# Kernel tuning notes

Hardware: AMD Instinct MI355X
Metric: run time of the kernel (lower is better)

## Reference

```python
import jax, jax.numpy as jnp
import numpy as np

RADIUS = 0.1
NUM_POINT = 1024  # M centroids
SAMPLE_NUM = 32   # K neighbors per ball


def fps(xyz, m):
    """D-FPS farthest point sampling. xyz: (B,N,3) -> idx (B,m) int32."""
    B, N, _ = xyz.shape

    def step(carry, _):
        mind, far = carry  # mind (B,N), far (B,)
        centroid = jnp.take_along_axis(xyz, far[:, None, None], axis=1)  # (B,1,3)
        d = jnp.sum((xyz - centroid) ** 2, axis=-1)  # (B,N)
        mind = jnp.minimum(mind, d)
        nxt = jnp.argmax(mind, axis=1).astype(jnp.int32)
        return (mind, nxt), far

    init = (jnp.full((B, N), jnp.inf, xyz.dtype), jnp.zeros((B,), jnp.int32))
    _, idx = jax.lax.scan(step, init, None, length=m)
    return jnp.transpose(idx)  # (B,m)


def ball_query(new_xyz, xyz, radius, k):
    """First-k points within radius of each centroid, padded with first hit.
    new_xyz (B,M,3), xyz (B,N,3) -> (B,M,k) int32."""
    N = xyz.shape[1]
    d2 = jnp.sum((new_xyz[:, :, None, :] - xyz[:, None, :, :]) ** 2, axis=-1)  # (B,M,N)
    order = jnp.where(d2 < radius * radius, jnp.arange(N, dtype=jnp.int32)[None, None, :], N)
    neg, pos = jax.lax.top_k(-order, k)  # k smallest 'order' values -> first-k in-ball indices
    valid = (-neg) < N
    return jnp.where(valid, pos, pos[..., :1])


def setup_inputs() -> dict:
    key = jax.random.key(0)
    ks = jax.random.split(key, 12)
    B, N, C = 4, 16384, 64
    Cin = C + 3  # use_xyz=True
    points_xyz = jax.random.uniform(ks[0], (B, N, 3), dtype=jnp.float32)
    features = jax.random.normal(ks[1], (B, C, N), dtype=jnp.float32)
    s = lambda fan: 1.0 / np.sqrt(fan)
    inp = {
        "points_xyz": points_xyz,
        "features": features,
        "Wa": jax.random.normal(ks[2], (128, Cin), jnp.float32) * s(Cin),
        "ba": jnp.zeros((128,), jnp.float32),
        "Wb": jax.random.normal(ks[3], (128, 128), jnp.float32) * s(128),
        "bb": jnp.zeros((128,), jnp.float32),
        "Ws": jax.random.normal(ks[4], (128, Cin), jnp.float32) * s(Cin),
        "bs": jnp.zeros((128,), jnp.float32),
        "Wc": jax.random.normal(ks[5], (512, 128), jnp.float32) * s(128),
        "bc": jnp.zeros((512,), jnp.float32),
        "Wd": jax.random.normal(ks[6], (128, 512), jnp.float32) * s(512),
        "bd": jnp.zeros((128,), jnp.float32),
    }
    return inp


def _conv1x1(W, b, x):
    # pointwise conv over (B,C,M,K)
    return jnp.einsum('oc,bcmk->bomk', W, x) + b[None, :, None, None]


def reference(points_xyz, features, Wa, ba, Wb, bb, Ws, bs, Wc, bc, Wd, bd):
    idx = fps(points_xyz, NUM_POINT)  # (B,M)
    new_xyz = jnp.take_along_axis(points_xyz, idx[:, :, None], axis=1)  # (B,M,3)
    nidx = ball_query(new_xyz, points_xyz, RADIUS, SAMPLE_NUM)  # (B,M,K)
    # gather and relativize grouped xyz; gather grouped features
    grouped_xyz = jax.vmap(lambda p, i: p[i])(points_xyz, nidx) - new_xyz[:, :, None, :]  # (B,M,K,3)
    gfeat = jax.vmap(lambda f, i: f[:, i])(features, nidx)  # (B,C,M,K)
    g = jnp.concatenate([jnp.transpose(grouped_xyz, (0, 3, 1, 2)), gfeat], axis=1)  # (B,3+C,M,K)
    # mlp + shortcut residual + relu
    h = _conv1x1(Wb, bb, jax.nn.relu(_conv1x1(Wa, ba, g)))
    h = jax.nn.relu(h + _conv1x1(Ws, bs, g))
    # inverted mlp + identity residual + relu
    inv = _conv1x1(Wd, bd, jax.nn.relu(_conv1x1(Wc, bc, h)))
    out = jax.nn.relu(inv + h)
    pooled = jnp.max(out, axis=-1)  # max pool over K -> (B,128,M)
    return new_xyz, pooled, idx
```

## Files before the change

kernel.cpp:

```cpp
#include <hip/hip_runtime.h>

#define N_PTS   16384
#define M_CENT  1024
#define K_SMP   32
#define C_FEAT  64
#define NCELL   512

using bf16x8 = __attribute__((ext_vector_type(8))) short;
using s16x4  = __attribute__((ext_vector_type(4))) short;
using f32x4  = __attribute__((ext_vector_type(4))) float;

__device__ inline short f2bf(float f) {
    unsigned u = __float_as_uint(f);
    u += 0x7fffu + ((u >> 16) & 1u);
    return (short)(u >> 16);
}

__device__ inline unsigned long long shfl_xor_u64(unsigned long long v, int m) {
    int lo = (int)(unsigned int)v;
    int hi = (int)(unsigned int)(v >> 32);
    lo = __shfl_xor(lo, m);
    hi = __shfl_xor(hi, m);
    return ((unsigned long long)(unsigned int)hi << 32) | (unsigned int)lo;
}

__device__ inline int part3(int v) {
    return (v & 1) | ((v & 2) << 2) | ((v & 4) << 4);
}
__device__ inline int cell_of(float x, float y, float z) {
    int xi = (int)(x * 8.0f); xi = xi < 0 ? 0 : (xi > 7 ? 7 : xi);
    int yi = (int)(y * 8.0f); yi = yi < 0 ? 0 : (yi > 7 ? 7 : yi);
    int zi = (int)(z * 8.0f); zi = zi < 0 ? 0 : (zi > 7 ? 7 : zi);
    return part3(xi) | (part3(yi) << 1) | (part3(zi) << 2);
}

__global__ __launch_bounds__(1024) void hist_kernel(
    const float* __restrict__ xyz, int* __restrict__ ghist)
{
    __shared__ int h[NCELL];
    const int b = blockIdx.x, tid = threadIdx.x;
    if (tid < NCELL) h[tid] = 0;
    __syncthreads();
    const float* P = xyz + (size_t)b * N_PTS * 3;
    for (int i = 0; i < 16; ++i) {
        const int p = tid + (i << 10);
        atomicAdd(&h[cell_of(P[p*3], P[p*3+1], P[p*3+2])], 1);
    }
    __syncthreads();
    if (tid < NCELL) ghist[b * NCELL + tid] = h[tid];
}

__global__ __launch_bounds__(NCELL) void scan_kernel(
    const int* __restrict__ ghist, int* __restrict__ gbase)
{
    __shared__ int h[NCELL];
    const int b = blockIdx.x, t = threadIdx.x;
    h[t] = ghist[b * NCELL + t];
    __syncthreads();
    int s = 0;
    for (int i = 0; i < t; ++i) s += h[i];
    gbase[b * NCELL + t] = s;
}

__global__ __launch_bounds__(1024) void scatter_kernel(
    const float* __restrict__ xyz, int* __restrict__ gbase,
    float4* __restrict__ gsxyz)
{
    const int b = blockIdx.x, tid = threadIdx.x;
    const float* P = xyz + (size_t)b * N_PTS * 3;
    for (int i = 0; i < 16; ++i) {
        const int p = tid + (i << 10);
        float x = P[p*3], y = P[p*3+1], z = P[p*3+2];
        int c = cell_of(x, y, z);
        int pos = atomicAdd(&gbase[b * NCELL + c], 1);
        gsxyz[(size_t)b * N_PTS + pos] = make_float4(x, y, z, __int_as_float(p));
    }
}

__global__ __launch_bounds__(1024) void fps_kernel(
    const float* __restrict__ xyz,
    const float4* __restrict__ gsxyz,
    float* __restrict__ newxyz_out,
    float* __restrict__ idxf_out)
{
#pragma clang fp contract(off)
    const int b = blockIdx.x, tid = threadIdx.x;
    const int wid = tid >> 6, lane = tid & 63;
    const float4* S = gsxyz + (size_t)b * N_PTS;

    float px[16], py[16], pz[16], mind[16];
    unsigned klo[16];
    float lox = 1e30f, hix = -1e30f, loy = 1e30f, hiy = -1e30f, loz = 1e30f, hiz = -1e30f;
#pragma unroll
    for (int i = 0; i < 16; ++i) {
        const float4 v = S[tid * 16 + i];
        px[i] = v.x; py[i] = v.y; pz[i] = v.z;
        const int orig = __float_as_int(v.w);
        klo[i] = ((unsigned)(16383 - orig) << 16) | (unsigned)(tid * 16 + i);
        mind[i] = __int_as_float(0x7f800000);
        lox = fminf(lox, v.x); hix = fmaxf(hix, v.x);
        loy = fminf(loy, v.y); hiy = fmaxf(hiy, v.y);
        loz = fminf(loz, v.z); hiz = fmaxf(hiz, v.z);
    }

    __shared__ unsigned long long wblk[2][16];

    const float* P = xyz + (size_t)b * N_PTS * 3;
    float cx = P[0], cy = P[1], cz = P[2];
    if (tid == 0) {
        idxf_out[b * M_CENT] = 0.0f;
        newxyz_out[(b * M_CENT) * 3 + 0] = cx;
        newxyz_out[(b * M_CENT) * 3 + 1] = cy;
        newxyz_out[(b * M_CENT) * 3 + 2] = cz;
    }
    __syncthreads();

    unsigned long long bkey = 0x7f80000000000000ull;
    unsigned long long wkey = 0x7f80000000000000ull;

    for (int j = 1; j < M_CENT; ++j) {
        const int par = j & 1;
        float tx = fmaxf(fmaxf(lox - cx, cx - hix), 0.0f);
        float ty = fmaxf(fmaxf(loy - cy, cy - hiy), 0.0f);
        float tz = fmaxf(fmaxf(loz - cz, cz - hiz), 0.0f);
        float lb = (tx * tx + ty * ty) + tz * tz;
        float lmax = __uint_as_float((unsigned)(bkey >> 32));
        bool need = (lb * 0.999985f) < lmax;

        if (__any(need)) {
            float bv = -1.0f;
#pragma unroll
            for (int i = 0; i < 16; ++i) {
                float dx = px[i] - cx;
                float dy = py[i] - cy;
                float dz = pz[i] - cz;
                float xx = dx * dx, yy = dy * dy, zz = dz * dz;
                float d  = (xx + yy) + zz;
                float mn = fminf(mind[i], d);
                mind[i] = mn;
                bv = fmaxf(bv, mn);
            }
            unsigned bk = 0u;
#pragma unroll
            for (int i = 0; i < 16; ++i)
                if (mind[i] == bv && klo[i] > bk) bk = klo[i];
            bkey = ((unsigned long long)__float_as_uint(bv) << 32) | bk;

            unsigned long long w = bkey;
#pragma unroll
            for (int off = 32; off >= 1; off >>= 1) {
                unsigned long long o = shfl_xor_u64(w, off);
                if (o > w) w = o;
            }
            wkey = w;
        }
        if (lane == 0) wblk[par][wid] = wkey;
        __syncthreads();

        unsigned long long k2 = wblk[par][lane & 15];
#pragma unroll
        for (int off = 8; off >= 1; off >>= 1) {
            unsigned long long o = shfl_xor_u64(k2, off);
            if (o > k2) k2 = o;
        }
        const unsigned int kl = (unsigned int)k2;
        const int sorted = (int)(kl & 0xFFFFu);
        const float4 wv = S[sorted];
        cx = wv.x; cy = wv.y; cz = wv.z;
        if (tid == 0) {
            const int orig = 16383 - (int)(kl >> 16);
            idxf_out[b * M_CENT + j] = (float)orig;
            newxyz_out[(b * M_CENT + j) * 3 + 0] = cx;
            newxyz_out[(b * M_CENT + j) * 3 + 1] = cy;
            newxyz_out[(b * M_CENT + j) * 3 + 2] = cz;
        }
    }
}

__global__ __launch_bounds__(256) void ball_kernel(
    const float* __restrict__ xyz,
    const float* __restrict__ newxyz,
    int* __restrict__ nidx)
{
#pragma clang fp contract(off)
    const float R2 = (float)(0.1 * 0.1);
    const int gw   = blockIdx.x * 4 + (threadIdx.x >> 6);
    const int lane = threadIdx.x & 63;
    const int b    = gw >> 10;
    const float* P = xyz + (size_t)b * N_PTS * 3;
    const float cx = newxyz[gw * 3 + 0];
    const float cy = newxyz[gw * 3 + 1];
    const float cz = newxyz[gw * 3 + 2];
    int* out = nidx + gw * K_SMP;

    int cnt = 0, first = -1;
    for (int base = 0; base < N_PTS; base += 64) {
        const int n = base + lane;
        float dx = P[n * 3 + 0] - cx;
        float dy = P[n * 3 + 1] - cy;
        float dz = P[n * 3 + 2] - cz;
        float xx = dx * dx, yy = dy * dy, zz = dz * dz;
        float d2 = (xx + yy) + zz;
        bool inb = d2 < R2;
        unsigned long long mask = __ballot(inb);
        if (mask) {
            if (first < 0) first = base + __ffsll(mask) - 1;
            int before = __popcll(mask & ((1ull << lane) - 1ull));
            int slot = cnt + before;
            if (inb && slot < K_SMP) out[slot] = n;
            cnt += __popcll(mask);
            if (cnt >= K_SMP) break;
        }
    }
    for (int s = cnt + lane; s < K_SMP; s += 64) out[s] = first;
}

__global__ void prep_w(const float* __restrict__ src, short* __restrict__ dst,
                       int OC, int IC, int ICP, int remap)
{
    int i = blockIdx.x * 256 + threadIdx.x;
    if (i >= OC * ICP) return;
    int oc = i / ICP, ic = i - oc * ICP;
    float v = 0.0f;
    if (remap) {
        if (ic < 64)      v = src[oc * IC + 3 + ic];
        else if (ic < 67) v = src[oc * IC + (ic - 64)];
    } else if (ic < IC)   v = src[oc * IC + ic];
    dst[i] = f2bf(v);
}

__global__ __launch_bounds__(256) void tfeat_kernel(
    const float* __restrict__ feat, float* __restrict__ featT)
{
    __shared__ float t[64][65];
    const int b = blockIdx.y;
    const int n0 = blockIdx.x * 64;
    for (int it = 0; it < 16; ++it) {
        int idx = it * 256 + threadIdx.x;
        int c = idx >> 6, n = idx & 63;
        t[c][n] = feat[((size_t)b * 64 + c) * N_PTS + n0 + n];
    }
    __syncthreads();
    for (int it = 0; it < 16; ++it) {
        int idx = it * 256 + threadIdx.x;
        int n = idx >> 6, c = idx & 63;
        featT[((size_t)b * N_PTS + n0 + n) * 64 + c] = t[c][n];
    }
}

__global__ __launch_bounds__(256, 2) void mlp_kernel(
    const float* __restrict__ xyz, const float* __restrict__ feat,
    const float* __restrict__ featT, int useT,
    const float* __restrict__ newxyz, const int* __restrict__ nidx,
    const short* __restrict__ WaB, const float* __restrict__ ba,
    const short* __restrict__ WbB, const float* __restrict__ bb,
    const short* __restrict__ WsB, const float* __restrict__ bs,
    const short* __restrict__ WcB, const float* __restrict__ bc,
    const short* __restrict__ WdB, const float* __restrict__ bd,
    float* __restrict__ pooled)
{
    __shared__ short Xt[64][104];
    __shared__ short Ht[64][136];
    __shared__ short Tt[64][136];

    const int tid = threadIdx.x;
    const int w = tid >> 6, l = tid & 63, l16 = l & 15, kg = l >> 4;
    const int cen0 = blockIdx.x * 2;
    const int b = cen0 >> 10;
    const int ocw = 32 * w;

    {
        const int col = tid >> 2, part = tid & 3;
        const int ci = cen0 + (col >> 5);
        const int nn = nidx[ci * K_SMP + (col & 31)];
        float v[16];
        if (useT) {
            const f32x4* src = (const f32x4*)(featT + ((size_t)b * N_PTS + nn) * 64 + part * 16);
            f32x4 f0 = src[0], f1 = src[1], f2 = src[2], f3 = src[3];
            v[0]=f0[0]; v[1]=f0[1]; v[2]=f0[2]; v[3]=f0[3];
            v[4]=f1[0]; v[5]=f1[1]; v[6]=f1[2]; v[7]=f1[3];
            v[8]=f2[0]; v[9]=f2[1]; v[10]=f2[2]; v[11]=f2[3];
            v[12]=f3[0]; v[13]=f3[1]; v[14]=f3[2]; v[15]=f3[3];
        } else {
            const float* F = feat + (size_t)b * C_FEAT * N_PTS + nn;
#pragma unroll
            for (int q = 0; q < 16; ++q) v[q] = F[(size_t)(part * 16 + q) * N_PTS];
        }
        bf16x8 h0, h1;
#pragma unroll
        for (int q = 0; q < 8; ++q) { h0[q] = f2bf(v[q]); h1[q] = f2bf(v[q + 8]); }
        *(bf16x8*)&Xt[col][part * 16]     = h0;
        *(bf16x8*)&Xt[col][part * 16 + 8] = h1;
        if (part == 0) {
            bf16x8 hx, z;
#pragma unroll
            for (int q = 0; q < 8; ++q) { hx[q] = 0; z[q] = 0; }
            hx[0] = f2bf(xyz[((size_t)b * N_PTS + nn) * 3 + 0] - newxyz[ci * 3 + 0]);
            hx[1] = f2bf(xyz[((size_t)b * N_PTS + nn) * 3 + 1] - newxyz[ci * 3 + 1]);
            hx[2] = f2bf(xyz[((size_t)b * N_PTS + nn) * 3 + 2] - newxyz[ci * 3 + 2]);
            *(bf16x8*)&Xt[col][64] = hx;
            *(bf16x8*)&Xt[col][72] = z;
            *(bf16x8*)&Xt[col][80] = z;
            *(bf16x8*)&Xt[col][88] = z;
        }
    }
    __syncthreads();

    f32x4 accA[2][4], accS[2][4];
#pragma unroll
    for (int o = 0; o < 2; ++o)
#pragma unroll
        for (int ct = 0; ct < 4; ++ct) {
#pragma unroll
            for (int r = 0; r < 4; ++r) { accA[o][ct][r] = 0.f; accS[o][ct][r] = 0.f; }
        }
#pragma unroll
    for (int k = 0; k < 3; ++k) {
        bf16x8 xb[4];
#pragma unroll
        for (int ct = 0; ct < 4; ++ct)
            xb[ct] = *(const bf16x8*)&Xt[ct * 16 + l16][k * 32 + kg * 8];
#pragma unroll
        for (int o = 0; o < 2; ++o) {
            const int row = ocw + o * 16 + l16;
            bf16x8 wa  = *(const bf16x8*)(WaB + row * 96 + k * 32 + kg * 8);
            bf16x8 wsv = *(const bf16x8*)(WsB + row * 96 + k * 32 + kg * 8);
#pragma unroll
            for (int ct = 0; ct < 4; ++ct) {
                accA[o][ct] = __builtin_amdgcn_mfma_f32_16x16x32_bf16(wa,  xb[ct], accA[o][ct], 0, 0, 0);
                accS[o][ct] = __builtin_amdgcn_mfma_f32_16x16x32_bf16(wsv, xb[ct], accS[o][ct], 0, 0, 0);
            }
        }
    }
#pragma unroll
    for (int o = 0; o < 2; ++o) {
        const f32x4 bav = *(const f32x4*)(ba + ocw + o * 16 + kg * 4);
#pragma unroll
        for (int ct = 0; ct < 4; ++ct) {
            s16x4 hv;
#pragma unroll
            for (int r = 0; r < 4; ++r) hv[r] = f2bf(fmaxf(accA[o][ct][r] + bav[r], 0.f));
            *(s16x4*)&Ht[ct * 16 + l16][ocw + o * 16 + kg * 4] = hv;
        }
    }
    __syncthreads();

    f32x4 accB[2][4];
#pragma unroll
    for (int o = 0; o < 2; ++o)
#pragma unroll
        for (int ct = 0; ct < 4; ++ct) {
#pragma unroll
            for (int r = 0; r < 4; ++r) accB[o][ct][r] = 0.f;
        }
#pragma unroll
    for (int k = 0; k < 4; ++k) {
        bf16x8 xb[4];
#pragma unroll
        for (int ct = 0; ct < 4; ++ct)
            xb[ct] = *(const bf16x8*)&Ht[ct * 16 + l16][k * 32 + kg * 8];
#pragma unroll
        for (int o = 0; o < 2; ++o) {
            const int row = ocw + o * 16 + l16;
            bf16x8 wbv = *(const bf16x8*)(WbB + row * 128 + k * 32 + kg * 8);
#pragma unroll
            for (int ct = 0; ct < 4; ++ct)
                accB[o][ct] = __builtin_amdgcn_mfma_f32_16x16x32_bf16(wbv, xb[ct], accB[o][ct], 0, 0, 0);
        }
    }
    f32x4 hreg[2][4];
#pragma unroll
    for (int o = 0; o < 2; ++o) {
        const f32x4 bbv = *(const f32x4*)(bb + ocw + o * 16 + kg * 4);
        const f32x4 bsv = *(const f32x4*)(bs + ocw + o * 16 + kg * 4);
#pragma unroll
        for (int ct = 0; ct < 4; ++ct) {
#pragma unroll
            for (int r = 0; r < 4; ++r)
                hreg[o][ct][r] = fmaxf((accB[o][ct][r] + bbv[r]) + (accS[o][ct][r] + bsv[r]), 0.f);
        }
    }
    __syncthreads();
#pragma unroll
    for (int o = 0; o < 2; ++o)
#pragma unroll
        for (int ct = 0; ct < 4; ++ct) {
            s16x4 hv;
#pragma unroll
            for (int r = 0; r < 4; ++r) hv[r] = f2bf(hreg[o][ct][r]);
            *(s16x4*)&Ht[ct * 16 + l16][ocw + o * 16 + kg * 4] = hv;
        }
    __syncthreads();

    f32x4 accD[2][4];
#pragma unroll
    for (int o = 0; o < 2; ++o)
#pragma unroll
        for (int ct = 0; ct < 4; ++ct) {
#pragma unroll
            for (int r = 0; r < 4; ++r) accD[o][ct][r] = 0.f;
        }
    for (int cc = 0; cc < 4; ++cc) {
        f32x4 accC[2][4];
#pragma unroll
        for (int o = 0; o < 2; ++o)
#pragma unroll
            for (int ct = 0; ct < 4; ++ct) {
#pragma unroll
                for (int r = 0; r < 4; ++r) accC[o][ct][r] = 0.f;
            }
#pragma unroll
        for (int k = 0; k < 4; ++k) {
            bf16x8 xb[4];
#pragma unroll
            for (int ct = 0; ct < 4; ++ct)
                xb[ct] = *(const bf16x8*)&Ht[ct * 16 + l16][k * 32 + kg * 8];
#pragma unroll
            for (int o = 0; o < 2; ++o) {
                const int row = cc * 128 + ocw + o * 16 + l16;
                bf16x8 wcv = *(const bf16x8*)(WcB + row * 128 + k * 32 + kg * 8);
#pragma unroll
                for (int ct = 0; ct < 4; ++ct)
                    accC[o][ct] = __builtin_amdgcn_mfma_f32_16x16x32_bf16(wcv, xb[ct], accC[o][ct], 0, 0, 0);
            }
        }
        __syncthreads();
#pragma unroll
        for (int o = 0; o < 2; ++o) {
            const f32x4 bcv = *(const f32x4*)(bc + cc * 128 + ocw + o * 16 + kg * 4);
#pragma unroll
            for (int ct = 0; ct < 4; ++ct) {
                s16x4 tv;
#pragma unroll
                for (int r = 0; r < 4; ++r) tv[r] = f2bf(fmaxf(accC[o][ct][r] + bcv[r], 0.f));
                *(s16x4*)&Tt[ct * 16 + l16][ocw + o * 16 + kg * 4] = tv;
            }
        }
        __syncthreads();
#pragma unroll
        for (int k = 0; k < 4; ++k) {
            bf16x8 tb[4];
#pragma unroll
            for (int ct = 0; ct < 4; ++ct)
                tb[ct] = *(const bf16x8*)&Tt[ct * 16 + l16][k * 32 + kg * 8];
#pragma unroll
            for (int o = 0; o < 2; ++o) {
                const int row = ocw + o * 16 + l16;
                bf16x8 wdv = *(const bf16x8*)(WdB + row * 512 + cc * 128 + k * 32 + kg * 8);
#pragma unroll
                for (int ct = 0; ct < 4; ++ct)
                    accD[o][ct] = __builtin_amdgcn_mfma_f32_16x16x32_bf16(wdv, tb[ct], accD[o][ct], 0, 0, 0);
            }
        }
    }

    const int m0 = cen0 & 1023;
#pragma unroll
    for (int o = 0; o < 2; ++o) {
        const f32x4 bdv = *(const f32x4*)(bd + ocw + o * 16 + kg * 4);
#pragma unroll
        for (int r = 0; r < 4; ++r) {
            float a0 = fmaxf((accD[o][0][r] + bdv[r]) + hreg[o][0][r], 0.f);
            float a1 = fmaxf((accD[o][1][r] + bdv[r]) + hreg[o][1][r], 0.f);
            float a2 = fmaxf((accD[o][2][r] + bdv[r]) + hreg[o][2][r], 0.f);
            float a3 = fmaxf((accD[o][3][r] + bdv[r]) + hreg[o][3][r], 0.f);
            float u0 = fmaxf(a0, a1), u1 = fmaxf(a2, a3);
#pragma unroll
            for (int off = 1; off < 16; off <<= 1) {
                u0 = fmaxf(u0, __shfl_xor(u0, off));
                u1 = fmaxf(u1, __shfl_xor(u1, off));
            }
            if (l16 == 0) {
                const int oc = ocw + o * 16 + kg * 4 + r;
                pooled[((size_t)b * 128 + oc) * 1024 + m0]     = u0;
                pooled[((size_t)b * 128 + oc) * 1024 + m0 + 1] = u1;
            }
        }
    }
}

extern "C" void kernel_launch(void* const* d_in, const int* in_sizes, int n_in,
                              void* d_out, int out_size, void* d_ws, size_t ws_size,
                              hipStream_t stream)
{
    const float* xyz  = (const float*)d_in[0];
    const float* feat = (const float*)d_in[1];
    const float* Wa = (const float*)d_in[2];   const float* ba = (const float*)d_in[3];
    const float* Wb = (const float*)d_in[4];   const float* bb = (const float*)d_in[5];
    const float* Ws = (const float*)d_in[6];   const float* bs = (const float*)d_in[7];
    const float* Wc = (const float*)d_in[8];   const float* bc = (const float*)d_in[9];
    const float* Wd = (const float*)d_in[10];  const float* bd = (const float*)d_in[11];

    float* out    = (float*)d_out;
    float* newxyz = out;
    float* pooled = out + 4 * 1024 * 3;
    float* idxf   = pooled + 4 * 128 * 1024;

    char* ws = (char*)d_ws;
    float4* gsxyz = (float4*)ws;
    int*    nidx  = (int*)ws;
    short* WaB = (short*)(ws + (1 << 20));
    short* WsB = WaB + 128 * 96;
    short* WbB = WsB + 128 * 96;
    short* WcB = WbB + 128 * 128;
    short* WdB = WcB + 512 * 128;
    int*   ghist = (int*)(WdB + 128 * 512);
    int*   gbase = ghist + 4 * NCELL;
    float* featT = (float*)(ws + (2 << 20));

    const size_t need = (size_t)(2 << 20) + (size_t)4 * N_PTS * 64 * 4;
    const int useT = (ws_size >= need) ? 1 : 0;

    prep_w<<<(128 *  96 + 255) / 256, 256, 0, stream>>>(Wa, WaB, 128,  67,  96, 1);
    prep_w<<<(128 *  96 + 255) / 256, 256, 0, stream>>>(Ws, WsB, 128,  67,  96, 1);
    prep_w<<<(128 * 128 + 255) / 256, 256, 0, stream>>>(Wb, WbB, 128, 128, 128, 0);
    prep_w<<<(512 * 128 + 255) / 256, 256, 0, stream>>>(Wc, WcB, 512, 128, 128, 0);
    prep_w<<<(128 * 512 + 255) / 256, 256, 0, stream>>>(Wd, WdB, 128, 512, 512, 0);
    if (useT) tfeat_kernel<<<dim3(N_PTS / 64, 4), 256, 0, stream>>>(feat, featT);

    hist_kernel   <<<4, 1024,  0, stream>>>(xyz, ghist);
    scan_kernel   <<<4, NCELL, 0, stream>>>(ghist, gbase);
    scatter_kernel<<<4, 1024,  0, stream>>>(xyz, gbase, gsxyz);

    fps_kernel<<<4, 1024, 0, stream>>>(xyz, gsxyz, newxyz, idxf);
    ball_kernel<<<1024, 256, 0, stream>>>(xyz, newxyz, nidx);
    mlp_kernel<<<2048, 256, 0, stream>>>(xyz, feat, featT, useT, newxyz, nidx,
                                         WaB, ba, WbB, bb, WsB, bs,
                                         WcB, bc, WdB, bd, pooled);
}
```

Baseline: 1.591 ms.

## Use Hilbert cell ordering and broadcast winner coords via shared memory in FPS

The spatial binning switches from Morton to Hilbert cell order, so the 16 points each thread owns are more compact and the bounding-box skip test triggers more often. In the FPS loop, the winning lane in each wave writes its key and coordinates to shared memory. The next centroid is then read from shared memory instead of a dependent global load of the sorted point buffer. This shortens the serial critical path per iteration, at the cost of extra selects in the argmax loop and more complex cell-index math in the binning kernels.

```diff
diff --git a/kernel.cpp b/kernel.cpp
--- a/kernel.cpp
+++ b/kernel.cpp
@@ -24,14 +24,31 @@
     return ((unsigned long long)(unsigned int)hi << 32) | (unsigned int)lo;
 }
 
-__device__ inline int part3(int v) {
-    return (v & 1) | ((v & 2) << 2) | ((v & 4) << 4);
-}
-__device__ inline int cell_of(float x, float y, float z) {
+__device__ inline int hcell_of(float x, float y, float z) {
     int xi = (int)(x * 8.0f); xi = xi < 0 ? 0 : (xi > 7 ? 7 : xi);
     int yi = (int)(y * 8.0f); yi = yi < 0 ? 0 : (yi > 7 ? 7 : yi);
     int zi = (int)(z * 8.0f); zi = zi < 0 ? 0 : (zi > 7 ? 7 : zi);
-    return part3(xi) | (part3(yi) << 1) | (part3(zi) << 2);
+    unsigned X[3] = {(unsigned)xi, (unsigned)yi, (unsigned)zi};
+#pragma unroll
+    for (unsigned Q = 4; Q > 1; Q >>= 1) {
+        unsigned P = Q - 1;
+#pragma unroll
+        for (int i = 0; i < 3; ++i) {
+            if (X[i] & Q) X[0] ^= P;
+            else { unsigned t = (X[0] ^ X[i]) & P; X[0] ^= t; X[i] ^= t; }
+        }
+    }
+    X[1] ^= X[0]; X[2] ^= X[1];
+    unsigned t = 0;
+#pragma unroll
+    for (unsigned Q = 4; Q > 1; Q >>= 1)
+        if (X[2] & Q) t ^= Q - 1;
+    X[0] ^= t; X[1] ^= t; X[2] ^= t;
+    int h = 0;
+#pragma unroll
+    for (int q = 2; q >= 0; --q)
+        h = (h << 3) | (((X[0] >> q) & 1) << 2) | (((X[1] >> q) & 1) << 1) | ((X[2] >> q) & 1);
+    return h;
 }
 
 __global__ __launch_bounds__(1024) void hist_kernel(
@@ -44,7 +61,7 @@
     const float* P = xyz + (size_t)b * N_PTS * 3;
     for (int i = 0; i < 16; ++i) {
         const int p = tid + (i << 10);
-        atomicAdd(&h[cell_of(P[p*3], P[p*3+1], P[p*3+2])], 1);
+        atomicAdd(&h[hcell_of(P[p*3], P[p*3+1], P[p*3+2])], 1);
     }
     __syncthreads();
     if (tid < NCELL) ghist[b * NCELL + tid] = h[tid];
@@ -71,7 +88,7 @@
     for (int i = 0; i < 16; ++i) {
         const int p = tid + (i << 10);
         float x = P[p*3], y = P[p*3+1], z = P[p*3+2];
-        int c = cell_of(x, y, z);
+        int c = hcell_of(x, y, z);
         int pos = atomicAdd(&gbase[b * NCELL + c], 1);
         gsxyz[(size_t)b * N_PTS + pos] = make_float4(x, y, z, __int_as_float(p));
     }
@@ -103,7 +120,8 @@
         loz = fminf(loz, v.z); hiz = fmaxf(hiz, v.z);
     }
 
-    __shared__ unsigned long long wblk[2][16];
+    __shared__ unsigned long long wkeys[2][16];
+    __shared__ float4 wcoord[2][16];
 
     const float* P = xyz + (size_t)b * N_PTS * 3;
     float cx = P[0], cy = P[1], cz = P[2];
@@ -117,6 +135,7 @@
 
     unsigned long long bkey = 0x7f80000000000000ull;
     unsigned long long wkey = 0x7f80000000000000ull;
+    float cwx = 0.f, cwy = 0.f, cwz = 0.f;
 
     for (int j = 1; j < M_CENT; ++j) {
         const int par = j & 1;
@@ -141,10 +160,17 @@
                 bv = fmaxf(bv, mn);
             }
             unsigned bk = 0u;
-#pragma unroll
-            for (int i = 0; i < 16; ++i)
-                if (mind[i] == bv && klo[i] > bk) bk = klo[i];
+            float wxx = 0.f, wyy = 0.f, wzz = 0.f;
+#pragma unroll
+            for (int i = 0; i < 16; ++i) {
+                bool c = (mind[i] == bv) && (klo[i] >= bk);
+                bk  = c ? klo[i] : bk;
+                wxx = c ? px[i]  : wxx;
+                wyy = c ? py[i]  : wyy;
+                wzz = c ? pz[i]  : wzz;
+            }
             bkey = ((unsigned long long)__float_as_uint(bv) << 32) | bk;
+            cwx = wxx; cwy = wyy; cwz = wzz;
 
             unsigned long long w = bkey;
 #pragma unroll
@@ -154,19 +180,22 @@
             }
             wkey = w;
         }
-        if (lane == 0) wblk[par][wid] = wkey;
+        if (bkey == wkey) {
+            wkeys[par][wid]  = wkey;
+            wcoord[par][wid] = make_float4(cwx, cwy, cwz, 0.f);
+        }
         __syncthreads();
 
-        unsigned long long k2 = wblk[par][lane & 15];
+        unsigned long long k2 = wkeys[par][lane & 15];
 #pragma unroll
         for (int off = 8; off >= 1; off >>= 1) {
             unsigned long long o = shfl_xor_u64(k2, off);
             if (o > k2) k2 = o;
         }
         const unsigned int kl = (unsigned int)k2;
-        const int sorted = (int)(kl & 0xFFFFu);
-        const float4 wv = S[sorted];
-        cx = wv.x; cy = wv.y; cz = wv.z;
+        const int winw = (int)((kl & 0xFFFFu) >> 10);
+        const float4 wc = wcoord[par][winw];
+        cx = wc.x; cy = wc.y; cz = wc.z;
         if (tid == 0) {
             const int orig = 16383 - (int)(kl >> 16);
             idxf_out[b * M_CENT + j] = (float)orig;
```

Result: slower. 2.548 ms (+60.1%).
